# Kernel tuning notes

Measured on AMD Instinct MI355X. Metric: run time of the kernel, lower is better.

Reference implementation:

```python
import jax, jax.numpy as jnp
import numpy as np

NUM_EXPERTS = 32
TOP_K = 4
HIDDEN = 2048
INTER = 768
N_TOKENS = 2048
NORM_TOPK = True


def setup_inputs() -> dict:
    key = jax.random.key(0)
    k0, k1, k2, k3 = jax.random.split(key, 4)
    hidden_states = jax.random.normal(k0, (N_TOKENS, HIDDEN), dtype=jnp.float32)
    # router gate: Linear(hidden, num_experts), stored as (h, E)
    Wg = jax.random.normal(k1, (HIDDEN, NUM_EXPERTS), dtype=jnp.float32) * 0.02
    # per-expert merged gate_up: (E, h, 2*i); down: (E, i, h)
    Wgu = jax.random.normal(k2, (NUM_EXPERTS, HIDDEN, 2 * INTER), dtype=jnp.float32) * 0.02
    Wd = jax.random.normal(k3, (NUM_EXPERTS, INTER, HIDDEN), dtype=jnp.float32) * 0.02
    return {"hidden_states": hidden_states, "Wg": Wg, "Wgu": Wgu, "Wd": Wd}


def reference(hidden_states, Wg, Wgu, Wd):
    E = Wgu.shape[0]
    # ---- routing ----
    router_logits = hidden_states @ Wg                       # (N, E)
    probs = jax.nn.softmax(router_logits.astype(jnp.float32), axis=-1)
    topk_w, topk_idx = jax.lax.top_k(probs, TOP_K)           # (N, K)
    if NORM_TOPK:
        topk_w = topk_w / jnp.sum(topk_w, axis=-1, keepdims=True)
    topk_w = topk_w.astype(hidden_states.dtype)
    # dense combine weights: (N, E), zero where expert not selected
    combine = jnp.einsum("nke,nk->ne", jax.nn.one_hot(topk_idx, E, dtype=topk_w.dtype), topk_w)
    # ---- experts (dense dispatch, zero-weighted combine == gather/scatter math) ----
    gate_up = jnp.einsum("nh,ehf->nef", hidden_states, Wgu)  # (N, E, 2i)
    gate, up = jnp.split(gate_up, 2, axis=-1)                # (N, E, i) each
    y = jax.nn.silu(gate) * up                               # SiluAndMul
    y = y * combine[:, :, None]                              # apply routing weight before down-proj (linear -> equivalent)
    out = jnp.einsum("nef,efh->nh", y, Wd)                   # (N, h)
    return out
```

## Files before the change

### kernel.cpp

```cpp
#include <hip/hip_runtime.h>
#include <hip/hip_bf16.h>

#define NE 32
#define TOPK 4
#define HID 2048
#define INTER 768
#define NT 2048
#define MAXTILE 96

typedef float f32x4 __attribute__((ext_vector_type(4)));
typedef unsigned int u32x4 __attribute__((ext_vector_type(4)));
typedef unsigned int u32x2 __attribute__((ext_vector_type(2)));
typedef short short8 __attribute__((ext_vector_type(8)));
typedef __bf16 bf16x8 __attribute__((ext_vector_type(8)));

__device__ inline unsigned short f2bf(float f) {
  unsigned u = __builtin_bit_cast(unsigned, f);
  u += 0x7fffu + ((u >> 16) & 1u);
  return (unsigned short)(u >> 16);
}
__device__ inline unsigned pack2(unsigned short a, unsigned short b) {
  return (unsigned)a | ((unsigned)b << 16);
}
__device__ inline f32x4 mfma_bf16(short8 a, short8 b, f32x4 c) {
  return __builtin_amdgcn_mfma_f32_16x16x32_bf16(
      __builtin_bit_cast(bf16x8, a), __builtin_bit_cast(bf16x8, b), c, 0, 0, 0);
}
__device__ inline void gload16(const void* g, void* l) {
  __builtin_amdgcn_global_load_lds(
      (const __attribute__((address_space(1))) void*)g,
      (__attribute__((address_space(3))) void*)l, 16, 0, 0);
}

__global__ __launch_bounds__(64) void k_router(const float* __restrict__ X,
                                               const float* __restrict__ Wg,
                                               int* __restrict__ expert_of,
                                               float* __restrict__ weight_of,
                                               int* __restrict__ counts) {
  const int n = blockIdx.x;
  const int lane = threadIdx.x;
  const float* x = X + (size_t)n * HID;
  float acc[NE];
#pragma unroll
  for (int e = 0; e < NE; ++e) acc[e] = 0.f;
  for (int h = lane; h < HID; h += 64) {
    const float xv = x[h];
    const f32x4* wr = (const f32x4*)(Wg + (size_t)h * NE);
#pragma unroll
    for (int q = 0; q < NE / 4; ++q) {
      f32x4 w4 = wr[q];
      acc[q * 4 + 0] += xv * w4[0];
      acc[q * 4 + 1] += xv * w4[1];
      acc[q * 4 + 2] += xv * w4[2];
      acc[q * 4 + 3] += xv * w4[3];
    }
  }
#pragma unroll
  for (int off = 32; off >= 1; off >>= 1) {
#pragma unroll
    for (int e = 0; e < NE; ++e) acc[e] += __shfl_xor(acc[e], off, 64);
  }
  if (lane == 0) {
    float m = acc[0];
#pragma unroll
    for (int e = 1; e < NE; ++e) m = fmaxf(m, acc[e]);
    unsigned used = 0;
    int idx[TOPK];
    float wv[TOPK];
    float wsum = 0.f;
    for (int k = 0; k < TOPK; ++k) {
      int best = 0;
      float bv = -1e30f;
      for (int e = 0; e < NE; ++e) {
        if (!((used >> e) & 1u) && acc[e] > bv) { bv = acc[e]; best = e; }
      }
      used |= 1u << best;
      float w = expf(bv - m);
      idx[k] = best;
      wv[k] = w;
      wsum += w;
    }
    const float inv = 1.f / wsum;
    for (int k = 0; k < TOPK; ++k) {
      expert_of[n * TOPK + k] = idx[k];
      weight_of[n * TOPK + k] = wv[k] * inv;
      atomicAdd(&counts[idx[k]], 1);
    }
  }
}

__global__ void k_scan(const int* __restrict__ counts, int* __restrict__ offsets,
                       int* __restrict__ wl_e, int* __restrict__ wl_m,
                       int* __restrict__ wl_n) {
  int s = 0, t = 0;
  for (int e = 0; e < NE; ++e) {
    offsets[e] = s;
    const int c = counts[e];
    for (int m0 = 0; m0 < c; m0 += 128) {
      wl_e[t] = e;
      wl_m[t] = m0;
      ++t;
    }
    s += c;
  }
  offsets[NE] = s;
  *wl_n = t;
}

__global__ __launch_bounds__(64) void k_scatter(const int* __restrict__ expert_of,
                                                const float* __restrict__ weight_of,
                                                const int* __restrict__ offsets,
                                                int* __restrict__ slot_token,
                                                float* __restrict__ slot_w) {
  const int e = blockIdx.x;
  const int lane = threadIdx.x;
  int cnt = offsets[e];
  for (int a0 = 0; a0 < NT * TOPK; a0 += 64) {
    const int a = a0 + lane;
    const bool m = (expert_of[a] == e);
    const unsigned long long bal = __ballot(m);
    if (m) {
      const int pos = cnt + __popcll(bal & ((1ull << lane) - 1ull));
      slot_token[pos] = a >> 2;
      slot_w[pos] = weight_of[a];
    }
    cnt += __popcll(bal);
  }
}

__global__ __launch_bounds__(256) void k_xconv(const float* __restrict__ X,
                                               unsigned short* __restrict__ Xb) {
  const int i = blockIdx.x * 256 + threadIdx.x;
  const f32x4 v = ((const f32x4*)X)[i];
  u32x2 t = {pack2(f2bf(v[0]), f2bf(v[1])), pack2(f2bf(v[2]), f2bf(v[3]))};
  ((u32x2*)Xb)[i] = t;
}

__global__ __launch_bounds__(256) void k_wconv(const float* __restrict__ W,
                                               unsigned short* __restrict__ WT,
                                               int K, int N) {
  const int e = blockIdx.z;
  const int k0 = blockIdx.x * 64;
  const int n0 = blockIdx.y * 64;
  __shared__ float T[64][65];
  const float* src = W + ((size_t)e * K + k0) * N + n0;
  const int t = threadIdx.x;
#pragma unroll
  for (int p = 0; p < 4; ++p) {
    const int q = p * 256 + t;
    const int r = q >> 4, c4 = q & 15;
    f32x4 v = *(const f32x4*)(src + (size_t)r * N + c4 * 4);
    T[r][c4 * 4 + 0] = v[0];
    T[r][c4 * 4 + 1] = v[1];
    T[r][c4 * 4 + 2] = v[2];
    T[r][c4 * 4 + 3] = v[3];
  }
  __syncthreads();
  unsigned short* dst = WT + ((size_t)e * N + n0) * K + k0;
#pragma unroll
  for (int p = 0; p < 2; ++p) {
    const int ch = p * 256 + t;
    const int n = ch >> 3, kc = ch & 7;
    __attribute__((aligned(16))) unsigned short tmp[8];
#pragma unroll
    for (int j = 0; j < 8; ++j) tmp[j] = f2bf(T[kc * 8 + j][n]);
    *(u32x4*)(dst + (size_t)n * K + kc * 8) = *(const u32x4*)tmp;
  }
}

__global__ __launch_bounds__(256) void k_gemm1(const unsigned short* __restrict__ Xb,
                                               const unsigned short* __restrict__ WguT,
                                               const int* __restrict__ slot_token,
                                               const float* __restrict__ slot_w,
                                               const int* __restrict__ offsets,
                                               const int* __restrict__ wl_e,
                                               const int* __restrict__ wl_m,
                                               const int* __restrict__ wl_n,
                                               unsigned short* __restrict__ Y) {
  const int tile = blockIdx.x;
  if (tile >= *wl_n) return;
  const int e = wl_e[tile];
  const int m0 = wl_m[tile];
  const int base = offsets[e];
  const int ne = offsets[e + 1] - base;
  const int n0 = blockIdx.y * 64;
  const int tid = threadIdx.x;
  const int lane = tid & 63, w = tid >> 6;
  const int wr = w >> 1, wc = w & 1;
  const int fr = lane & 15, fo = lane >> 4;
  const int lr = lane >> 3, lk = lane & 7;

  __shared__ __attribute__((aligned(16))) unsigned short As[128 * 64];
  __shared__ __attribute__((aligned(16))) unsigned short Bg[64 * 64];
  __shared__ __attribute__((aligned(16))) unsigned short Bu[64 * 64];

  f32x4 accg[4][2], accu[4][2];
#pragma unroll
  for (int i = 0; i < 4; ++i)
#pragma unroll
    for (int j = 0; j < 2; ++j) {
      f32x4 z = {0.f, 0.f, 0.f, 0.f};
      accg[i][j] = z;
      accu[i][j] = z;
    }

  const unsigned short* asrc[4];
#pragma unroll
  for (int i = 0; i < 4; ++i) {
    const int ra = (w * 4 + i) * 8 + lr;
    const int tok = slot_token[base + min(m0 + ra, ne - 1)];
    asrc[i] = Xb + (size_t)tok * HID + ((lk ^ (ra & 7)) << 3);
  }
  const unsigned short* gsrc[2];
  const unsigned short* usrc[2];
#pragma unroll
  for (int j = 0; j < 2; ++j) {
    const int rb = (w * 2 + j) * 8 + lr;
    gsrc[j] = WguT + ((size_t)e * (2 * INTER) + n0 + rb) * HID + ((lk ^ (rb & 7)) << 3);
    usrc[j] = WguT + ((size_t)e * (2 * INTER) + INTER + n0 + rb) * HID + ((lk ^ (rb & 7)) << 3);
  }

  for (int k0 = 0; k0 < HID; k0 += 64) {
#pragma unroll
    for (int i = 0; i < 4; ++i) gload16(asrc[i] + k0, &As[(w * 4 + i) * 512]);
#pragma unroll
    for (int j = 0; j < 2; ++j) {
      gload16(gsrc[j] + k0, &Bg[(w * 2 + j) * 512]);
      gload16(usrc[j] + k0, &Bu[(w * 2 + j) * 512]);
    }
    __syncthreads();
#pragma unroll
    for (int ks = 0; ks < 2; ++ks) {
      const int c = ks * 4 + fo;
      short8 a[4], bg[2], bu[2];
#pragma unroll
      for (int mi = 0; mi < 4; ++mi) {
        const int row = wr * 64 + mi * 16 + fr;
        a[mi] = *(const short8*)&As[row * 64 + ((c ^ (row & 7)) << 3)];
      }
#pragma unroll
      for (int ni = 0; ni < 2; ++ni) {
        const int row = wc * 32 + ni * 16 + fr;
        const int off = row * 64 + ((c ^ (row & 7)) << 3);
        bg[ni] = *(const short8*)&Bg[off];
        bu[ni] = *(const short8*)&Bu[off];
      }
#pragma unroll
      for (int mi = 0; mi < 4; ++mi)
#pragma unroll
        for (int ni = 0; ni < 2; ++ni) {
          accg[mi][ni] = mfma_bf16(a[mi], bg[ni], accg[mi][ni]);
          accu[mi][ni] = mfma_bf16(a[mi], bu[ni], accu[mi][ni]);
        }
    }
    __syncthreads();
  }

#pragma unroll
  for (int mi = 0; mi < 4; ++mi) {
#pragma unroll
    for (int j = 0; j < 4; ++j) {
      const int gm = m0 + wr * 64 + mi * 16 + fo * 4 + j;
      if (gm < ne) {
        const float wgt = slot_w[base + gm];
        unsigned short* yp = Y + (size_t)(base + gm) * INTER + n0 + wc * 32;
#pragma unroll
        for (int ni = 0; ni < 2; ++ni) {
          const float g = accg[mi][ni][j];
          const float u = accu[mi][ni][j];
          const float yv = (g / (1.0f + __expf(-g))) * u * wgt;
          yp[ni * 16 + fr] = f2bf(yv);
        }
      }
    }
  }
}

__global__ __launch_bounds__(256) void k_gemm2(const unsigned short* __restrict__ Y,
                                               const unsigned short* __restrict__ WdT,
                                               const int* __restrict__ slot_token,
                                               const int* __restrict__ offsets,
                                               const int* __restrict__ wl_e,
                                               const int* __restrict__ wl_m,
                                               const int* __restrict__ wl_n,
                                               float* __restrict__ out) {
  const int tile = blockIdx.x;
  if (tile >= *wl_n) return;
  const int e = wl_e[tile];
  const int m0 = wl_m[tile];
  const int base = offsets[e];
  const int ne = offsets[e + 1] - base;
  const int n0 = blockIdx.y * 128;
  const int tid = threadIdx.x;
  const int lane = tid & 63, w = tid >> 6;
  const int wr = w >> 1, wc = w & 1;
  const int fr = lane & 15, fo = lane >> 4;
  const int lr = lane >> 3, lk = lane & 7;

  __shared__ __attribute__((aligned(16))) unsigned short As[128 * 64];
  __shared__ __attribute__((aligned(16))) unsigned short Bs[128 * 64];

  f32x4 acc[4][4];
#pragma unroll
  for (int i = 0; i < 4; ++i)
#pragma unroll
    for (int j = 0; j < 4; ++j) {
      f32x4 z = {0.f, 0.f, 0.f, 0.f};
      acc[i][j] = z;
    }

  const unsigned short* asrc[4];
  const unsigned short* bsrc[4];
#pragma unroll
  for (int i = 0; i < 4; ++i) {
    const int ra = (w * 4 + i) * 8 + lr;
    const int grow = base + min(m0 + ra, ne - 1);
    asrc[i] = Y + (size_t)grow * INTER + ((lk ^ (ra & 7)) << 3);
    bsrc[i] = WdT + ((size_t)e * HID + n0 + ra) * INTER + ((lk ^ (ra & 7)) << 3);
  }

  for (int k0 = 0; k0 < INTER; k0 += 64) {
#pragma unroll
    for (int i = 0; i < 4; ++i) {
      gload16(asrc[i] + k0, &As[(w * 4 + i) * 512]);
      gload16(bsrc[i] + k0, &Bs[(w * 4 + i) * 512]);
    }
    __syncthreads();
#pragma unroll
    for (int ks = 0; ks < 2; ++ks) {
      const int c = ks * 4 + fo;
      short8 a[4], b[4];
#pragma unroll
      for (int mi = 0; mi < 4; ++mi) {
        const int row = wr * 64 + mi * 16 + fr;
        a[mi] = *(const short8*)&As[row * 64 + ((c ^ (row & 7)) << 3)];
      }
#pragma unroll
      for (int ni = 0; ni < 4; ++ni) {
        const int row = wc * 64 + ni * 16 + fr;
        b[ni] = *(const short8*)&Bs[row * 64 + ((c ^ (row & 7)) << 3)];
      }
#pragma unroll
      for (int mi = 0; mi < 4; ++mi)
#pragma unroll
        for (int ni = 0; ni < 4; ++ni) acc[mi][ni] = mfma_bf16(a[mi], b[ni], acc[mi][ni]);
    }
    __syncthreads();
  }

#pragma unroll
  for (int mi = 0; mi < 4; ++mi) {
#pragma unroll
    for (int j = 0; j < 4; ++j) {
      const int gm = m0 + wr * 64 + mi * 16 + fo * 4 + j;
      if (gm < ne) {
        const int tok = slot_token[base + gm];
        float* op = out + (size_t)tok * HID + n0 + wc * 64;
#pragma unroll
        for (int ni = 0; ni < 4; ++ni) atomicAdd(&op[ni * 16 + fr], acc[mi][ni][j]);
      }
    }
  }
}

extern "C" void kernel_launch(void* const* d_in, const int* in_sizes, int n_in,
                              void* d_out, int out_size, void* d_ws, size_t ws_size,
                              hipStream_t stream) {
  (void)in_sizes; (void)n_in; (void)ws_size;
  const float* X = (const float*)d_in[0];
  const float* Wg = (const float*)d_in[1];
  const float* Wgu = (const float*)d_in[2];
  const float* Wd = (const float*)d_in[3];
  float* out = (float*)d_out;

  char* ws = (char*)d_ws;
  int* counts = (int*)(ws + 0);
  int* offsets = (int*)(ws + 256);
  int* wl_n = (int*)(ws + 512);
  int* wl_e = (int*)(ws + 1024);
  int* wl_m = (int*)(ws + 1536);
  int* expert_of = (int*)(ws + 2048);
  float* weight_of = (float*)(ws + 2048 + 32768);
  int* slot_token = (int*)(ws + 2048 + 2 * 32768);
  float* slot_w = (float*)(ws + 2048 + 3 * 32768);
  unsigned short* Xb = (unsigned short*)(ws + 133120);
  unsigned short* Yb = (unsigned short*)(ws + 8521728);
  unsigned short* WguT = (unsigned short*)(ws + 21104640);
  unsigned short* WdT = (unsigned short*)(ws + 222431232);

  hipMemsetAsync(counts, 0, 128, stream);
  hipMemsetAsync(d_out, 0, (size_t)out_size * sizeof(float), stream);

  k_router<<<NT, 64, 0, stream>>>(X, Wg, expert_of, weight_of, counts);
  k_scan<<<1, 1, 0, stream>>>(counts, offsets, wl_e, wl_m, wl_n);
  k_scatter<<<NE, 64, 0, stream>>>(expert_of, weight_of, offsets, slot_token, slot_w);
  k_xconv<<<(NT * HID / 4) / 256, 256, 0, stream>>>(X, Xb);
  k_wconv<<<dim3(HID / 64, (2 * INTER) / 64, NE), 256, 0, stream>>>(Wgu, WguT, HID, 2 * INTER);
  k_wconv<<<dim3(INTER / 64, HID / 64, NE), 256, 0, stream>>>(Wd, WdT, INTER, HID);
  k_gemm1<<<dim3(MAXTILE, INTER / 64), 256, 0, stream>>>(Xb, WguT, slot_token, slot_w,
                                                         offsets, wl_e, wl_m, wl_n, Yb);
  k_gemm2<<<dim3(MAXTILE, HID / 128), 256, 0, stream>>>(Yb, WdT, slot_token, offsets,
                                                        wl_e, wl_m, wl_n, out);
}
```

Baseline: 593.0 us.

## Fuse fp32 weight conversion into grouped GEMMs and enlarge M tile to 256

Removes the separate weight transpose/convert kernels and has both grouped GEMMs read fp32 expert weights directly, converting them to bf16 and writing them transposed into swizzled shared memory. This avoids writing and re-reading roughly 300MB of converted weights per call. Blocks grow to 512 threads with a 256-row token tile, which halves the work-list granularity and the number of times weights are re-read per expert. The cost is twice the bytes per weight load, register-staged loads instead of async direct-to-LDS copies, and more padding waste for experts with few tokens.

```diff
diff --git a/kernel.cpp b/kernel.cpp
--- a/kernel.cpp
+++ b/kernel.cpp
@@ -6,9 +6,10 @@
 #define HID 2048
 #define INTER 768
 #define NT 2048
-#define MAXTILE 96
+#define MAXTILE 64
 
 typedef float f32x4 __attribute__((ext_vector_type(4)));
+typedef float f32x2 __attribute__((ext_vector_type(2)));
 typedef unsigned int u32x4 __attribute__((ext_vector_type(4)));
 typedef unsigned int u32x2 __attribute__((ext_vector_type(2)));
 typedef short short8 __attribute__((ext_vector_type(8)));
@@ -96,7 +97,7 @@
   for (int e = 0; e < NE; ++e) {
     offsets[e] = s;
     const int c = counts[e];
-    for (int m0 = 0; m0 < c; m0 += 128) {
+    for (int m0 = 0; m0 < c; m0 += 256) {
       wl_e[t] = e;
       wl_m[t] = m0;
       ++t;
@@ -136,40 +137,8 @@
   ((u32x2*)Xb)[i] = t;
 }
 
-__global__ __launch_bounds__(256) void k_wconv(const float* __restrict__ W,
-                                               unsigned short* __restrict__ WT,
-                                               int K, int N) {
-  const int e = blockIdx.z;
-  const int k0 = blockIdx.x * 64;
-  const int n0 = blockIdx.y * 64;
-  __shared__ float T[64][65];
-  const float* src = W + ((size_t)e * K + k0) * N + n0;
-  const int t = threadIdx.x;
-#pragma unroll
-  for (int p = 0; p < 4; ++p) {
-    const int q = p * 256 + t;
-    const int r = q >> 4, c4 = q & 15;
-    f32x4 v = *(const f32x4*)(src + (size_t)r * N + c4 * 4);
-    T[r][c4 * 4 + 0] = v[0];
-    T[r][c4 * 4 + 1] = v[1];
-    T[r][c4 * 4 + 2] = v[2];
-    T[r][c4 * 4 + 3] = v[3];
-  }
-  __syncthreads();
-  unsigned short* dst = WT + ((size_t)e * N + n0) * K + k0;
-#pragma unroll
-  for (int p = 0; p < 2; ++p) {
-    const int ch = p * 256 + t;
-    const int n = ch >> 3, kc = ch & 7;
-    __attribute__((aligned(16))) unsigned short tmp[8];
-#pragma unroll
-    for (int j = 0; j < 8; ++j) tmp[j] = f2bf(T[kc * 8 + j][n]);
-    *(u32x4*)(dst + (size_t)n * K + kc * 8) = *(const u32x4*)tmp;
-  }
-}
-
-__global__ __launch_bounds__(256) void k_gemm1(const unsigned short* __restrict__ Xb,
-                                               const unsigned short* __restrict__ WguT,
+__global__ __launch_bounds__(512) void k_gemm1(const unsigned short* __restrict__ Xb,
+                                               const float* __restrict__ Wgu,
                                                const int* __restrict__ slot_token,
                                                const float* __restrict__ slot_w,
                                                const int* __restrict__ offsets,
@@ -186,11 +155,11 @@
   const int n0 = blockIdx.y * 64;
   const int tid = threadIdx.x;
   const int lane = tid & 63, w = tid >> 6;
-  const int wr = w >> 1, wc = w & 1;
+  const int wm = w >> 1, wn = w & 1;
   const int fr = lane & 15, fo = lane >> 4;
   const int lr = lane >> 3, lk = lane & 7;
 
-  __shared__ __attribute__((aligned(16))) unsigned short As[128 * 64];
+  __shared__ __attribute__((aligned(16))) unsigned short As[256 * 64];
   __shared__ __attribute__((aligned(16))) unsigned short Bg[64 * 64];
   __shared__ __attribute__((aligned(16))) unsigned short Bu[64 * 64];
 
@@ -211,23 +180,28 @@
     const int tok = slot_token[base + min(m0 + ra, ne - 1)];
     asrc[i] = Xb + (size_t)tok * HID + ((lk ^ (ra & 7)) << 3);
   }
-  const unsigned short* gsrc[2];
-  const unsigned short* usrc[2];
-#pragma unroll
-  for (int j = 0; j < 2; ++j) {
-    const int rb = (w * 2 + j) * 8 + lr;
-    gsrc[j] = WguT + ((size_t)e * (2 * INTER) + n0 + rb) * HID + ((lk ^ (rb & 7)) << 3);
-    usrc[j] = WguT + ((size_t)e * (2 * INTER) + INTER + n0 + rb) * HID + ((lk ^ (rb & 7)) << 3);
-  }
+
+  const int np = tid & 31, kg = (tid >> 5) & 7, rg = tid >> 8;
+  const float* bsrc = Wgu + (size_t)e * HID * (2 * INTER) + (size_t)(kg * 8) * (2 * INTER) +
+                      rg * INTER + n0 + 2 * np;
+  unsigned short* Bd = rg ? Bu : Bg;
+  const int n_a = 2 * np, n_b = 2 * np + 1;
+  const int wofa = n_a * 64 + ((kg ^ (n_a & 7)) << 3);
+  const int wofb = n_b * 64 + ((kg ^ (n_b & 7)) << 3);
 
   for (int k0 = 0; k0 < HID; k0 += 64) {
 #pragma unroll
     for (int i = 0; i < 4; ++i) gload16(asrc[i] + k0, &As[(w * 4 + i) * 512]);
-#pragma unroll
-    for (int j = 0; j < 2; ++j) {
-      gload16(gsrc[j] + k0, &Bg[(w * 2 + j) * 512]);
-      gload16(usrc[j] + k0, &Bu[(w * 2 + j) * 512]);
-    }
+    const float* bp = bsrc + (size_t)k0 * (2 * INTER);
+    f32x2 bv[8];
+#pragma unroll
+    for (int j = 0; j < 8; ++j) bv[j] = *(const f32x2*)(bp + (size_t)j * (2 * INTER));
+    u32x4 ta = {pack2(f2bf(bv[0][0]), f2bf(bv[1][0])), pack2(f2bf(bv[2][0]), f2bf(bv[3][0])),
+                pack2(f2bf(bv[4][0]), f2bf(bv[5][0])), pack2(f2bf(bv[6][0]), f2bf(bv[7][0]))};
+    u32x4 tb = {pack2(f2bf(bv[0][1]), f2bf(bv[1][1])), pack2(f2bf(bv[2][1]), f2bf(bv[3][1])),
+                pack2(f2bf(bv[4][1]), f2bf(bv[5][1])), pack2(f2bf(bv[6][1]), f2bf(bv[7][1]))};
+    *(u32x4*)&Bd[wofa] = ta;
+    *(u32x4*)&Bd[wofb] = tb;
     __syncthreads();
 #pragma unroll
     for (int ks = 0; ks < 2; ++ks) {
@@ -235,12 +209,12 @@
       short8 a[4], bg[2], bu[2];
 #pragma unroll
       for (int mi = 0; mi < 4; ++mi) {
-        const int row = wr * 64 + mi * 16 + fr;
+        const int row = wm * 64 + mi * 16 + fr;
         a[mi] = *(const short8*)&As[row * 64 + ((c ^ (row & 7)) << 3)];
       }
 #pragma unroll
       for (int ni = 0; ni < 2; ++ni) {
-        const int row = wc * 32 + ni * 16 + fr;
+        const int row = wn * 32 + ni * 16 + fr;
         const int off = row * 64 + ((c ^ (row & 7)) << 3);
         bg[ni] = *(const short8*)&Bg[off];
         bu[ni] = *(const short8*)&Bu[off];
@@ -260,10 +234,10 @@
   for (int mi = 0; mi < 4; ++mi) {
 #pragma unroll
     for (int j = 0; j < 4; ++j) {
-      const int gm = m0 + wr * 64 + mi * 16 + fo * 4 + j;
+      const int gm = m0 + wm * 64 + mi * 16 + fo * 4 + j;
       if (gm < ne) {
         const float wgt = slot_w[base + gm];
-        unsigned short* yp = Y + (size_t)(base + gm) * INTER + n0 + wc * 32;
+        unsigned short* yp = Y + (size_t)(base + gm) * INTER + n0 + wn * 32;
 #pragma unroll
         for (int ni = 0; ni < 2; ++ni) {
           const float g = accg[mi][ni][j];
@@ -276,8 +250,8 @@
   }
 }
 
-__global__ __launch_bounds__(256) void k_gemm2(const unsigned short* __restrict__ Y,
-                                               const unsigned short* __restrict__ WdT,
+__global__ __launch_bounds__(512) void k_gemm2(const unsigned short* __restrict__ Y,
+                                               const float* __restrict__ Wd,
                                                const int* __restrict__ slot_token,
                                                const int* __restrict__ offsets,
                                                const int* __restrict__ wl_e,
@@ -293,11 +267,11 @@
   const int n0 = blockIdx.y * 128;
   const int tid = threadIdx.x;
   const int lane = tid & 63, w = tid >> 6;
-  const int wr = w >> 1, wc = w & 1;
+  const int wm = w >> 1, wn = w & 1;
   const int fr = lane & 15, fo = lane >> 4;
   const int lr = lane >> 3, lk = lane & 7;
 
-  __shared__ __attribute__((aligned(16))) unsigned short As[128 * 64];
+  __shared__ __attribute__((aligned(16))) unsigned short As[256 * 64];
   __shared__ __attribute__((aligned(16))) unsigned short Bs[128 * 64];
 
   f32x4 acc[4][4];
@@ -310,21 +284,32 @@
     }
 
   const unsigned short* asrc[4];
-  const unsigned short* bsrc[4];
 #pragma unroll
   for (int i = 0; i < 4; ++i) {
     const int ra = (w * 4 + i) * 8 + lr;
     const int grow = base + min(m0 + ra, ne - 1);
     asrc[i] = Y + (size_t)grow * INTER + ((lk ^ (ra & 7)) << 3);
-    bsrc[i] = WdT + ((size_t)e * HID + n0 + ra) * INTER + ((lk ^ (ra & 7)) << 3);
-  }
+  }
+
+  const int np = tid & 63, kg = tid >> 6;
+  const float* bsrc = Wd + (size_t)e * INTER * HID + (size_t)(kg * 8) * HID + n0 + 2 * np;
+  const int n_a = 2 * np, n_b = 2 * np + 1;
+  const int wofa = n_a * 64 + ((kg ^ (n_a & 7)) << 3);
+  const int wofb = n_b * 64 + ((kg ^ (n_b & 7)) << 3);
 
   for (int k0 = 0; k0 < INTER; k0 += 64) {
 #pragma unroll
-    for (int i = 0; i < 4; ++i) {
-      gload16(asrc[i] + k0, &As[(w * 4 + i) * 512]);
-      gload16(bsrc[i] + k0, &Bs[(w * 4 + i) * 512]);
-    }
+    for (int i = 0; i < 4; ++i) gload16(asrc[i] + k0, &As[(w * 4 + i) * 512]);
+    const float* bp = bsrc + (size_t)k0 * HID;
+    f32x2 bv[8];
+#pragma unroll
+    for (int j = 0; j < 8; ++j) bv[j] = *(const f32x2*)(bp + (size_t)j * HID);
+    u32x4 ta = {pack2(f2bf(bv[0][0]), f2bf(bv[1][0])), pack2(f2bf(bv[2][0]), f2bf(bv[3][0])),
+                pack2(f2bf(bv[4][0]), f2bf(bv[5][0])), pack2(f2bf(bv[6][0]), f2bf(bv[7][0]))};
+    u32x4 tb = {pack2(f2bf(bv[0][1]), f2bf(bv[1][1])), pack2(f2bf(bv[2][1]), f2bf(bv[3][1])),
+                pack2(f2bf(bv[4][1]), f2bf(bv[5][1])), pack2(f2bf(bv[6][1]), f2bf(bv[7][1]))};
+    *(u32x4*)&Bs[wofa] = ta;
+    *(u32x4*)&Bs[wofb] = tb;
     __syncthreads();
 #pragma unroll
     for (int ks = 0; ks < 2; ++ks) {
@@ -332,12 +317,12 @@
       short8 a[4], b[4];
 #pragma unroll
       for (int mi = 0; mi < 4; ++mi) {
-        const int row = wr * 64 + mi * 16 + fr;
+        const int row = wm * 64 + mi * 16 + fr;
         a[mi] = *(const short8*)&As[row * 64 + ((c ^ (row & 7)) << 3)];
       }
 #pragma unroll
       for (int ni = 0; ni < 4; ++ni) {
-        const int row = wc * 64 + ni * 16 + fr;
+        const int row = wn * 64 + ni * 16 + fr;
         b[ni] = *(const short8*)&Bs[row * 64 + ((c ^ (row & 7)) << 3)];
       }
 #pragma unroll
@@ -352,10 +337,10 @@
   for (int mi = 0; mi < 4; ++mi) {
 #pragma unroll
     for (int j = 0; j < 4; ++j) {
-      const int gm = m0 + wr * 64 + mi * 16 + fo * 4 + j;
+      const int gm = m0 + wm * 64 + mi * 16 + fo * 4 + j;
       if (gm < ne) {
         const int tok = slot_token[base + gm];
-        float* op = out + (size_t)tok * HID + n0 + wc * 64;
+        float* op = out + (size_t)tok * HID + n0 + wn * 64;
 #pragma unroll
         for (int ni = 0; ni < 4; ++ni) atomicAdd(&op[ni * 16 + fr], acc[mi][ni][j]);
       }
@@ -385,8 +370,6 @@
   float* slot_w = (float*)(ws + 2048 + 3 * 32768);
   unsigned short* Xb = (unsigned short*)(ws + 133120);
   unsigned short* Yb = (unsigned short*)(ws + 8521728);
-  unsigned short* WguT = (unsigned short*)(ws + 21104640);
-  unsigned short* WdT = (unsigned short*)(ws + 222431232);
 
   hipMemsetAsync(counts, 0, 128, stream);
   hipMemsetAsync(d_out, 0, (size_t)out_size * sizeof(float), stream);
@@ -395,10 +378,8 @@
   k_scan<<<1, 1, 0, stream>>>(counts, offsets, wl_e, wl_m, wl_n);
   k_scatter<<<NE, 64, 0, stream>>>(expert_of, weight_of, offsets, slot_token, slot_w);
   k_xconv<<<(NT * HID / 4) / 256, 256, 0, stream>>>(X, Xb);
-  k_wconv<<<dim3(HID / 64, (2 * INTER) / 64, NE), 256, 0, stream>>>(Wgu, WguT, HID, 2 * INTER);
-  k_wconv<<<dim3(INTER / 64, HID / 64, NE), 256, 0, stream>>>(Wd, WdT, INTER, HID);
-  k_gemm1<<<dim3(MAXTILE, INTER / 64), 256, 0, stream>>>(Xb, WguT, slot_token, slot_w,
+  k_gemm1<<<dim3(MAXTILE, INTER / 64), 512, 0, stream>>>(Xb, Wgu, slot_token, slot_w,
                                                          offsets, wl_e, wl_m, wl_n, Yb);
-  k_gemm2<<<dim3(MAXTILE, HID / 128), 256, 0, stream>>>(Yb, WdT, slot_token, offsets,
+  k_gemm2<<<dim3(MAXTILE, HID / 128), 512, 0, stream>>>(Yb, Wd, slot_token, offsets,
                                                         wl_e, wl_m, wl_n, out);
 }
```

After: 481.8 us. 1.23x faster.
